# Performance work log

Measured on AMD Instinct MI355X. Metric: run time of the kernel, lower is better.

Reference implementation:

```python
import jax, jax.numpy as jnp
import numpy as np

SIGMA = 1.0
MAX_RADIUS = 3.0
EPS = 1e-08


def setup_inputs() -> dict:
    key = jax.random.key(0)
    k1, k2 = jax.random.split(key)
    z_generated = jax.random.normal(k1, (2048, 512), dtype=jnp.float32)
    z_known = jax.random.normal(k2, (32768, 512), dtype=jnp.float32)
    return {"z_generated": z_generated, "z_known": z_known}


def _cdist(x, y):
    # Euclidean pairwise distances [B, K] via the expanded quadratic form.
    x2 = jnp.sum(x * x, axis=-1, keepdims=True)          # [B, 1]
    y2 = jnp.sum(y * y, axis=-1, keepdims=True).T        # [1, K]
    d2 = x2 + y2 - 2.0 * jnp.einsum('bd,kd->bk', x, y)   # [B, K]
    return jnp.sqrt(jnp.maximum(d2, 0.0))


def reference(z_generated, z_known):
    dists = _cdist(z_generated, z_known)                 # [B, K]
    w_sigma = jnp.exp(-(dists ** 2) / (SIGMA ** 2))      # RBF weights
    w_sum = jnp.sum(w_sigma, axis=1, keepdims=True) + EPS
    w_norm = w_sigma / w_sum
    soft_distance = jnp.sum(w_norm * dists, axis=1)      # [B]
    capped = jnp.minimum(soft_distance, MAX_RADIUS)
    return -jnp.mean(capped)
```

## Files before the change

kernel.cpp:

```cpp
#include <hip/hip_runtime.h>
#include <stdint.h>

#define D_DIM 512
#define DB 256
#define MAX_RADIUS 3.0f
#define EPS 1e-8f

#define EXP_CUTOFF 104.0f

#define BN 64
#define NSUB 8
#define NG (NSUB * 2)

typedef int i32x4 __attribute__((ext_vector_type(4)));
typedef int i32x8 __attribute__((ext_vector_type(8)));
typedef float f32x16 __attribute__((ext_vector_type(16)));

#define GLOBAL_AS __attribute__((address_space(1)))
#define LDS_AS __attribute__((address_space(3)))

static __device__ __forceinline__ i32x8 cat4z(i32x4 lo) {
  i32x8 v;
  v[0] = lo[0]; v[1] = lo[1]; v[2] = lo[2]; v[3] = lo[3];
  v[4] = 0; v[5] = 0; v[6] = 0; v[7] = 0;
  return v;
}

__global__ void zero_out(float* out) {
  if (threadIdx.x == 0 && blockIdx.x == 0) out[0] = 0.0f;
}

__global__ __launch_bounds__(256) void convert_fp4_both(
    const float* __restrict__ X, const float* __restrict__ Y,
    uint8_t* __restrict__ Xf, uint8_t* __restrict__ Yf,
    float* __restrict__ x2, float* __restrict__ y2,
    float* __restrict__ za, float* __restrict__ zb, int M, int N) {
  int wid = threadIdx.x >> 6;
  int lane = threadIdx.x & 63;
  int row = blockIdx.x * 4 + wid;
  if (row >= M + N) return;
  bool isX = row < M;
  const float* src = isX ? (X + (size_t)row * D_DIM) : (Y + (size_t)(row - M) * D_DIM);
  const float4* s4 = reinterpret_cast<const float4*>(src + lane * 8);
  float4 a = s4[0], b = s4[1];
  float v[8] = {a.x, a.y, a.z, a.w, b.x, b.y, b.z, b.w};
  float ss = 0.f;
  uint32_t pack = 0;
#pragma unroll
  for (int j = 0; j < 8; ++j) {
    ss = fmaf(v[j], v[j], ss);
    union { float f; uint32_t u; } bits; bits.f = v[j];
    float u = fabsf(v[j]);
    uint32_t code = (uint32_t)(u > 0.25f) + (uint32_t)(u > 0.75f) +
                    (uint32_t)(u > 1.25f) + (uint32_t)(u > 1.75f) +
                    (uint32_t)(u > 2.5f)  + (uint32_t)(u > 3.5f)  +
                    (uint32_t)(u > 5.0f);
    code |= (bits.u >> 31) << 3;
    pack |= code << (4 * j);
  }
  uint8_t* dst = isX ? (Xf + (size_t)row * DB) : (Yf + (size_t)(row - M) * DB);
  reinterpret_cast<uint32_t*>(dst)[lane] = pack;
#pragma unroll
  for (int s = 1; s < 64; s <<= 1) ss += __shfl_xor(ss, s, 64);
  if (lane == 0) {
    if (isX) { x2[row] = ss; za[row] = 0.0f; zb[row] = 0.0f; }
    else     { y2[row - M] = ss; }
  }
}

__global__ __launch_bounds__(128, 2) void gemm_fp4(
    const uint8_t* __restrict__ Yf, const uint8_t* __restrict__ Xf,
    const float* __restrict__ y2, const float* __restrict__ x2,
    float* __restrict__ wsum, float* __restrict__ wdsum, int Mtiles, int Ngrps) {
  __shared__ __align__(16) uint8_t smem[32768];

  int nwg = Mtiles * Ngrps;
  int bid = blockIdx.x;
  int swz = bid;
  if ((nwg & 7) == 0) {
    int chunk = nwg >> 3;
    swz = (bid & 7) * chunk + (bid >> 3);
  }
  int mt = swz % Mtiles;
  int ng = swz / Mtiles;
  int m0 = mt * BN;

  int tid = threadIdx.x;
  int lane = tid & 63;
  int wid = tid >> 6;
  int lr = lane & 31, lh = lane >> 5;
  int nw0 = ng * 1024 + wid * 512;

#pragma unroll
  for (int i = 0; i < 8; ++i) {
    int rowl = i * 8 + (tid >> 4);
    int lc = (tid & 15) ^ (rowl & 15);
    __builtin_amdgcn_global_load_lds(
        (const GLOBAL_AS uint32_t*)(Xf + (size_t)(m0 + rowl) * DB + lc * 16),
        (LDS_AS uint32_t*)&smem[i * 2048 + tid * 16], 16, 0, 0);
  }

  float y2m[NSUB];
#pragma unroll
  for (int s = 0; s < NSUB; ++s) {
    float yv = y2[nw0 + s * 64 + lane];
#pragma unroll
    for (int q = 1; q < 64; q <<= 1) yv = fminf(yv, __shfl_xor(yv, q, 64));
    y2m[s] = yv;
  }
  float x2m0 = x2[m0 + lr];
  float x2m1 = x2[m0 + 32 + lr];

  asm volatile("s_waitcnt vmcnt(0)" ::: "memory");
  __syncthreads();

  i32x4 bq[8][2];
#pragma unroll
  for (int w = 0; w < 8; ++w)
#pragma unroll
    for (int f = 0; f < 2; ++f) {
      int row = f * 32 + lr;
      int cs = ((2 * w + lh) ^ (lr & 15)) * 16;
      bq[w][f] = *(const i32x4*)&smem[row * DB + cs];
    }
  __syncthreads();

  uint8_t* Yw = &smem[wid * 16384];
  const uint8_t* gY0 = Yf + (size_t)(nw0 + (lane >> 3)) * DB
                          + (((lane & 7) ^ ((lane >> 3) & 7)) * 16);

#define STAGE(g)                                                                              \
  do {                                                                                        \
    const uint8_t* s_ = gY0 + (size_t)((g) >> 1) * (64 * DB) + ((g) & 1) * 128;               \
    uint8_t* d_ = Yw + ((g) & 1) * 8192 + lane * 16;                                          \
    _Pragma("unroll")                                                                         \
    for (int i_ = 0; i_ < 8; ++i_)                                                            \
      __builtin_amdgcn_global_load_lds((const GLOBAL_AS uint32_t*)(s_ + (size_t)i_ * 8 * DB), \
                                       (LDS_AS uint32_t*)(d_ + i_ * 1024), 16, 0, 0);         \
  } while (0)

  STAGE(0);
  STAGE(1);

  int cs0 = ((0 + lh) ^ (lr & 7)) * 16;
  int cs1 = ((2 + lh) ^ (lr & 7)) * 16;
  int cs2 = ((4 + lh) ^ (lr & 7)) * 16;
  int cs3 = ((6 + lh) ^ (lr & 7)) * 16;

  f32x16 acc00, acc01, acc10, acc11;
#pragma unroll
  for (int r = 0; r < 16; ++r) { acc00[r] = 0.f; acc01[r] = 0.f; acc10[r] = 0.f; acc11[r] = 0.f; }

#pragma unroll
  for (int s = 0; s < NSUB; ++s) {
#pragma unroll
    for (int t = 0; t < 2; ++t) {
      const int g = s * 2 + t;
      if (g + 2 < NG) STAGE(g + 2);
      if (g + 2 < NG)       { asm volatile("s_waitcnt vmcnt(16)" ::: "memory"); }
      else if (g + 1 < NG)  { asm volatile("s_waitcnt vmcnt(8)"  ::: "memory"); }
      else                  { asm volatile("s_waitcnt vmcnt(0)"  ::: "memory"); }

      const uint8_t* A = Yw + (g & 1) * 8192;
      i32x4 f00 = *(const i32x4*)(A + lr * 128 + cs0);
      i32x4 f01 = *(const i32x4*)(A + (32 + lr) * 128 + cs0);
      i32x4 f10 = *(const i32x4*)(A + lr * 128 + cs1);
      i32x4 f11 = *(const i32x4*)(A + (32 + lr) * 128 + cs1);
      i32x4 f20 = *(const i32x4*)(A + lr * 128 + cs2);
      i32x4 f21 = *(const i32x4*)(A + (32 + lr) * 128 + cs2);
      i32x4 f30 = *(const i32x4*)(A + lr * 128 + cs3);
      i32x4 f31 = *(const i32x4*)(A + (32 + lr) * 128 + cs3);
      int w0 = t * 4;
      __builtin_amdgcn_s_setprio(1);
      acc00 = __builtin_amdgcn_mfma_scale_f32_32x32x64_f8f6f4(cat4z(f00), cat4z(bq[w0][0]), acc00, 4, 4, 0, 127, 0, 127);
      acc01 = __builtin_amdgcn_mfma_scale_f32_32x32x64_f8f6f4(cat4z(f00), cat4z(bq[w0][1]), acc01, 4, 4, 0, 127, 0, 127);
      acc10 = __builtin_amdgcn_mfma_scale_f32_32x32x64_f8f6f4(cat4z(f01), cat4z(bq[w0][0]), acc10, 4, 4, 0, 127, 0, 127);
      acc11 = __builtin_amdgcn_mfma_scale_f32_32x32x64_f8f6f4(cat4z(f01), cat4z(bq[w0][1]), acc11, 4, 4, 0, 127, 0, 127);
      acc00 = __builtin_amdgcn_mfma_scale_f32_32x32x64_f8f6f4(cat4z(f10), cat4z(bq[w0 + 1][0]), acc00, 4, 4, 0, 127, 0, 127);
      acc01 = __builtin_amdgcn_mfma_scale_f32_32x32x64_f8f6f4(cat4z(f10), cat4z(bq[w0 + 1][1]), acc01, 4, 4, 0, 127, 0, 127);
      acc10 = __builtin_amdgcn_mfma_scale_f32_32x32x64_f8f6f4(cat4z(f11), cat4z(bq[w0 + 1][0]), acc10, 4, 4, 0, 127, 0, 127);
      acc11 = __builtin_amdgcn_mfma_scale_f32_32x32x64_f8f6f4(cat4z(f11), cat4z(bq[w0 + 1][1]), acc11, 4, 4, 0, 127, 0, 127);
      acc00 = __builtin_amdgcn_mfma_scale_f32_32x32x64_f8f6f4(cat4z(f20), cat4z(bq[w0 + 2][0]), acc00, 4, 4, 0, 127, 0, 127);
      acc01 = __builtin_amdgcn_mfma_scale_f32_32x32x64_f8f6f4(cat4z(f20), cat4z(bq[w0 + 2][1]), acc01, 4, 4, 0, 127, 0, 127);
      acc10 = __builtin_amdgcn_mfma_scale_f32_32x32x64_f8f6f4(cat4z(f21), cat4z(bq[w0 + 2][0]), acc10, 4, 4, 0, 127, 0, 127);
      acc11 = __builtin_amdgcn_mfma_scale_f32_32x32x64_f8f6f4(cat4z(f21), cat4z(bq[w0 + 2][1]), acc11, 4, 4, 0, 127, 0, 127);
      acc00 = __builtin_amdgcn_mfma_scale_f32_32x32x64_f8f6f4(cat4z(f30), cat4z(bq[w0 + 3][0]), acc00, 4, 4, 0, 127, 0, 127);
      acc01 = __builtin_amdgcn_mfma_scale_f32_32x32x64_f8f6f4(cat4z(f30), cat4z(bq[w0 + 3][1]), acc01, 4, 4, 0, 127, 0, 127);
      acc10 = __builtin_amdgcn_mfma_scale_f32_32x32x64_f8f6f4(cat4z(f31), cat4z(bq[w0 + 3][0]), acc10, 4, 4, 0, 127, 0, 127);
      acc11 = __builtin_amdgcn_mfma_scale_f32_32x32x64_f8f6f4(cat4z(f31), cat4z(bq[w0 + 3][1]), acc11, 4, 4, 0, 127, 0, 127);
      __builtin_amdgcn_s_setprio(0);
    }

    int n0s = nw0 + s * 64;
#pragma unroll
    for (int fj = 0; fj < 2; ++fj) {
      int m = m0 + fj * 32 + lr;
      float x2v = fj ? x2m1 : x2m0;
      const f32x16& a0 = fj ? acc01 : acc00;
      const f32x16& a1 = fj ? acc11 : acc10;
      float cmax = a0[0];
#pragma unroll
      for (int r = 0; r < 16; ++r) cmax = fmaxf(cmax, fmaxf(a0[r], a1[r]));
      bool maybe = (x2v + y2m[s] - 2.0f * cmax) < EXP_CUTOFF;
      if (__any(maybe)) {
        float wsp = 0.f, wdp = 0.f;
#pragma unroll
        for (int fi = 0; fi < 2; ++fi) {
#pragma unroll
          for (int r = 0; r < 16; ++r) {
            int n = n0s + fi * 32 + (r & 3) + 8 * (r >> 2) + 4 * lh;
            float c = fi ? a1[r] : a0[r];
            float d2 = fmaxf(x2v + y2[n] - 2.0f * c, 0.0f);
            if (d2 < EXP_CUTOFF) {
              float d = sqrtf(d2);
              float w = __expf(-d2);
              wsp += w;
              wdp = fmaf(w, d, wdp);
            }
          }
        }
        wsp += __shfl_xor(wsp, 32, 64);
        wdp += __shfl_xor(wdp, 32, 64);
        if (lh == 0) {
          atomicAdd(&wsum[m], wsp);
          atomicAdd(&wdsum[m], wdp);
        }
      }
    }
    if (s < NSUB - 1) {
#pragma unroll
      for (int r = 0; r < 16; ++r) { acc00[r] = 0.f; acc01[r] = 0.f; acc10[r] = 0.f; acc11[r] = 0.f; }
    }
  }
#undef STAGE
}

__global__ __launch_bounds__(256) void finalize(const float* __restrict__ wsum,
                                                const float* __restrict__ wdsum,
                                                float* __restrict__ out, int M) {
  __shared__ float red[256];
  float acc = 0.f;
  for (int r = threadIdx.x; r < M; r += 256) {
    float soft = wdsum[r] / (wsum[r] + EPS);
    acc += fminf(soft, MAX_RADIUS);
  }
  red[threadIdx.x] = acc;
  __syncthreads();
  for (int s = 128; s > 0; s >>= 1) {
    if (threadIdx.x < s) red[threadIdx.x] += red[threadIdx.x + s];
    __syncthreads();
  }
  if (threadIdx.x == 0) out[0] = -red[0] / (float)M;
}

__global__ __launch_bounds__(256) void fallback_row(const float* __restrict__ X,
                                                    const float* __restrict__ Y,
                                                    float* __restrict__ out, int M, int N) {
  __shared__ float xs[D_DIM];
  __shared__ float red[512];
  int b = blockIdx.x;
  for (int i = threadIdx.x; i < D_DIM; i += 256) xs[i] = X[(size_t)b * D_DIM + i];
  __syncthreads();
  float ws = 0.f, wd = 0.f;
  for (int k = threadIdx.x; k < N; k += 256) {
    const float4* y4 = reinterpret_cast<const float4*>(Y + (size_t)k * D_DIM);
    float d2 = 0.f;
#pragma unroll 8
    for (int j = 0; j < D_DIM / 4; ++j) {
      float4 yv = y4[j];
      float4 xv = *reinterpret_cast<const float4*>(&xs[j * 4]);
      float dx = xv.x - yv.x, dy = xv.y - yv.y, dz = xv.z - yv.z, dw = xv.w - yv.w;
      d2 += dx * dx + dy * dy + dz * dz + dw * dw;
    }
    if (d2 < EXP_CUTOFF) {
      float d = sqrtf(d2);
      float w = __expf(-d2);
      ws += w; wd = fmaf(w, d, wd);
    }
  }
  red[threadIdx.x] = ws; red[256 + threadIdx.x] = wd;
  __syncthreads();
  for (int s = 128; s > 0; s >>= 1) {
    if (threadIdx.x < s) {
      red[threadIdx.x] += red[threadIdx.x + s];
      red[256 + threadIdx.x] += red[256 + threadIdx.x + s];
    }
    __syncthreads();
  }
  if (threadIdx.x == 0) {
    float soft = red[256] / (red[0] + EPS);
    atomicAdd(out, -fminf(soft, MAX_RADIUS) / (float)M);
  }
}

extern "C" void kernel_launch(void* const* d_in, const int* in_sizes, int n_in,
                              void* d_out, int out_size, void* d_ws, size_t ws_size,
                              hipStream_t stream) {
  const float* X = (const float*)d_in[0];
  const float* Y = (const float*)d_in[1];
  float* out = (float*)d_out;
  int M = in_sizes[0] / D_DIM;
  int N = in_sizes[1] / D_DIM;

  auto align256 = [](size_t x) { return (x + 255) & ~(size_t)255; };
  size_t oXf = 0;
  size_t oYf = align256(oXf + (size_t)M * DB);
  size_t ox2 = align256(oYf + (size_t)N * DB);
  size_t oy2 = align256(ox2 + (size_t)M * 4);
  size_t ows = align256(oy2 + (size_t)N * 4);
  size_t owd = align256(ows + (size_t)M * 4);
  size_t need = owd + (size_t)M * 4;

  bool fast = (ws_size >= need) && (M % BN == 0) && (N % 1024 == 0);
  if (fast) {
    char* ws = (char*)d_ws;
    uint8_t* Xf = (uint8_t*)(ws + oXf);
    uint8_t* Yf = (uint8_t*)(ws + oYf);
    float* x2 = (float*)(ws + ox2);
    float* y2 = (float*)(ws + oy2);
    float* wsv = (float*)(ws + ows);
    float* wdv = (float*)(ws + owd);

    convert_fp4_both<<<(M + N + 3) / 4, 256, 0, stream>>>(X, Y, Xf, Yf, x2, y2, wsv, wdv, M, N);
    int Mtiles = M / BN, Ngrps = N / 1024;
    gemm_fp4<<<Mtiles * Ngrps, 128, 0, stream>>>(Yf, Xf, y2, x2, wsv, wdv, Mtiles, Ngrps);
    finalize<<<1, 256, 0, stream>>>(wsv, wdv, out, M);
  } else {
    zero_out<<<1, 64, 0, stream>>>(out);
    fallback_row<<<M, 256, 0, stream>>>(X, Y, out, M, N);
  }
}
```

Baseline: 46.06 us.

## Share Y tiles across four waves via LDS triple-buffer ring with barriers

Restructures the fp4 GEMM tiling. Each workgroup now has four waves, each owning a different 64-row slice of X, and all four share a single stream of 512 Y rows staged through a three-slot LDS ring that is synchronized with barriers. Previously each wave streamed its own Y rows into a private double buffer. X fragments are now loaded straight from global memory into registers, with no LDS round trip. The aim is to cut Y global and LDS traffic per unit of MFMA work and to reduce LDS footprint, at the cost of per-stage workgroup barriers and smaller per-wave loads.

Result: faster. 43.12 us (-6.4%).

```diff
diff --git a/kernel.cpp b/kernel.cpp
--- a/kernel.cpp
+++ b/kernel.cpp
@@ -8,7 +8,7 @@
 
 #define EXP_CUTOFF 104.0f
 
-#define BN 64
+#define BN 256
 #define NSUB 8
 #define NG (NSUB * 2)
 
@@ -68,11 +68,11 @@
   }
 }
 
-__global__ __launch_bounds__(128, 2) void gemm_fp4(
+__global__ __launch_bounds__(256, 2) void gemm_fp4(
     const uint8_t* __restrict__ Yf, const uint8_t* __restrict__ Xf,
     const float* __restrict__ y2, const float* __restrict__ x2,
     float* __restrict__ wsum, float* __restrict__ wdsum, int Mtiles, int Ngrps) {
-  __shared__ __align__(16) uint8_t smem[32768];
+  __shared__ __align__(16) uint8_t ring[3 * 8192];
 
   int nwg = Mtiles * Ngrps;
   int bid = blockIdx.x;
@@ -89,16 +89,15 @@
   int lane = tid & 63;
   int wid = tid >> 6;
   int lr = lane & 31, lh = lane >> 5;
-  int nw0 = ng * 1024 + wid * 512;
-
-#pragma unroll
-  for (int i = 0; i < 8; ++i) {
-    int rowl = i * 8 + (tid >> 4);
-    int lc = (tid & 15) ^ (rowl & 15);
-    __builtin_amdgcn_global_load_lds(
-        (const GLOBAL_AS uint32_t*)(Xf + (size_t)(m0 + rowl) * DB + lc * 16),
-        (LDS_AS uint32_t*)&smem[i * 2048 + tid * 16], 16, 0, 0);
-  }
+  int mw0 = m0 + wid * 64;
+  int nw0 = ng * (NSUB * 64);
+
+  i32x4 bq[8][2];
+#pragma unroll
+  for (int w = 0; w < 8; ++w)
+#pragma unroll
+    for (int f = 0; f < 2; ++f)
+      bq[w][f] = *(const i32x4*)(Xf + (size_t)(mw0 + f * 32 + lr) * DB + (2 * w + lh) * 16);
 
   float y2m[NSUB];
 #pragma unroll
@@ -108,35 +107,21 @@
     for (int q = 1; q < 64; q <<= 1) yv = fminf(yv, __shfl_xor(yv, q, 64));
     y2m[s] = yv;
   }
-  float x2m0 = x2[m0 + lr];
-  float x2m1 = x2[m0 + 32 + lr];
-
-  asm volatile("s_waitcnt vmcnt(0)" ::: "memory");
-  __syncthreads();
-
-  i32x4 bq[8][2];
-#pragma unroll
-  for (int w = 0; w < 8; ++w)
-#pragma unroll
-    for (int f = 0; f < 2; ++f) {
-      int row = f * 32 + lr;
-      int cs = ((2 * w + lh) ^ (lr & 15)) * 16;
-      bq[w][f] = *(const i32x4*)&smem[row * DB + cs];
-    }
-  __syncthreads();
-
-  uint8_t* Yw = &smem[wid * 16384];
-  const uint8_t* gY0 = Yf + (size_t)(nw0 + (lane >> 3)) * DB
-                          + (((lane & 7) ^ ((lane >> 3) & 7)) * 16);
+  float x2m0 = x2[mw0 + lr];
+  float x2m1 = x2[mw0 + 32 + lr];
+
+  int rbase = (tid >> 6) * 8 + ((tid >> 3) & 7);
+  int lc = (tid & 7) ^ ((tid >> 3) & 7);
+  const uint8_t* gY0 = Yf + (size_t)(nw0 + rbase) * DB + lc * 16;
 
 #define STAGE(g)                                                                              \
   do {                                                                                        \
     const uint8_t* s_ = gY0 + (size_t)((g) >> 1) * (64 * DB) + ((g) & 1) * 128;               \
-    uint8_t* d_ = Yw + ((g) & 1) * 8192 + lane * 16;                                          \
-    _Pragma("unroll")                                                                         \
-    for (int i_ = 0; i_ < 8; ++i_)                                                            \
-      __builtin_amdgcn_global_load_lds((const GLOBAL_AS uint32_t*)(s_ + (size_t)i_ * 8 * DB), \
-                                       (LDS_AS uint32_t*)(d_ + i_ * 1024), 16, 0, 0);         \
+    uint8_t* d_ = ring + ((g) % 3) * 8192 + tid * 16;                                         \
+    __builtin_amdgcn_global_load_lds((const GLOBAL_AS uint32_t*)(s_),                         \
+                                     (LDS_AS uint32_t*)(d_), 16, 0, 0);                       \
+    __builtin_amdgcn_global_load_lds((const GLOBAL_AS uint32_t*)(s_ + 32 * DB),               \
+                                     (LDS_AS uint32_t*)(d_ + 4096), 16, 0, 0);                \
   } while (0)
 
   STAGE(0);
@@ -156,12 +141,13 @@
 #pragma unroll
     for (int t = 0; t < 2; ++t) {
       const int g = s * 2 + t;
+      if (g < NG - 1) { asm volatile("s_waitcnt vmcnt(2)" ::: "memory"); }
+      else            { asm volatile("s_waitcnt vmcnt(0)" ::: "memory"); }
+      __builtin_amdgcn_s_barrier();
+      __builtin_amdgcn_sched_barrier(0);
       if (g + 2 < NG) STAGE(g + 2);
-      if (g + 2 < NG)       { asm volatile("s_waitcnt vmcnt(16)" ::: "memory"); }
-      else if (g + 1 < NG)  { asm volatile("s_waitcnt vmcnt(8)"  ::: "memory"); }
-      else                  { asm volatile("s_waitcnt vmcnt(0)"  ::: "memory"); }
-
-      const uint8_t* A = Yw + (g & 1) * 8192;
+
+      const uint8_t* A = ring + (g % 3) * 8192;
       i32x4 f00 = *(const i32x4*)(A + lr * 128 + cs0);
       i32x4 f01 = *(const i32x4*)(A + (32 + lr) * 128 + cs0);
       i32x4 f10 = *(const i32x4*)(A + lr * 128 + cs1);
@@ -194,7 +180,7 @@
     int n0s = nw0 + s * 64;
 #pragma unroll
     for (int fj = 0; fj < 2; ++fj) {
-      int m = m0 + fj * 32 + lr;
+      int m = mw0 + fj * 32 + lr;
       float x2v = fj ? x2m1 : x2m0;
       const f32x16& a0 = fj ? acc01 : acc00;
       const f32x16& a1 = fj ? acc11 : acc10;
@@ -311,7 +297,7 @@
   size_t owd = align256(ows + (size_t)M * 4);
   size_t need = owd + (size_t)M * 4;
 
-  bool fast = (ws_size >= need) && (M % BN == 0) && (N % 1024 == 0);
+  bool fast = (ws_size >= need) && (M % BN == 0) && (N % (NSUB * 64) == 0);
   if (fast) {
     char* ws = (char*)d_ws;
     uint8_t* Xf = (uint8_t*)(ws + oXf);
@@ -322,8 +308,8 @@
     float* wdv = (float*)(ws + owd);
 
     convert_fp4_both<<<(M + N + 3) / 4, 256, 0, stream>>>(X, Y, Xf, Yf, x2, y2, wsv, wdv, M, N);
-    int Mtiles = M / BN, Ngrps = N / 1024;
-    gemm_fp4<<<Mtiles * Ngrps, 128, 0, stream>>>(Yf, Xf, y2, x2, wsv, wdv, Mtiles, Ngrps);
+    int Mtiles = M / BN, Ngrps = N / (NSUB * 64);
+    gemm_fp4<<<Mtiles * Ngrps, 256, 0, stream>>>(Yf, Xf, y2, x2, wsv, wdv, Mtiles, Ngrps);
     finalize<<<1, 256, 0, stream>>>(wsv, wdv, out, M);
   } else {
     zero_out<<<1, 64, 0, stream>>>(out);
```
